# Kernel tuning notes

Measured on AMD Instinct MI355X. Metric: run time of the kernel, lower is better.

The kernel has to match this reference:

```python
import jax, jax.numpy as jnp
import numpy as np

N_NODES = 50000
N_EDGES = 800000
IN_C, H0, H1, OUT_C = 64, 64, 64, 16
EPS = 1e-5


def _sage_min(x, src, dst, Wl, bl, Wr, n_nodes):
    # PyG SAGEConv(aggr='min'): out = lin_l(min_{j in N(i)} x_j) + lin_r(x_i)
    agg = jax.ops.segment_min(x[src], dst, num_segments=n_nodes)
    agg = jnp.where(jnp.isfinite(agg), agg, 0.0)  # empty segments -> 0 (torch_scatter default)
    return agg @ Wl + bl + x @ Wr


def _batchnorm(x, gamma, beta):
    # training-mode BatchNorm1d over node dim, biased variance, eps=1e-5
    mu = jnp.mean(x, axis=0)
    var = jnp.mean((x - mu) ** 2, axis=0)
    return gamma * (x - mu) * jax.lax.rsqrt(var + EPS) + beta


def setup_inputs() -> dict:
    key = jax.random.key(0)
    ks = jax.random.split(key, 16)
    x = jax.random.normal(ks[0], (N_NODES, IN_C), dtype=jnp.float32)
    edge_index = jax.random.randint(ks[1], (2, N_EDGES), 0, N_NODES, dtype=jnp.int64)

    def lin(k, fan_in, fan_out):
        s = 1.0 / np.sqrt(fan_in)
        return jax.random.uniform(k, (fan_in, fan_out), jnp.float32, -s, s)

    return {
        "x": x, "edge_index": edge_index,
        "W1l": lin(ks[2], IN_C, H0), "b1": jnp.zeros((H0,), jnp.float32), "W1r": lin(ks[3], IN_C, H0),
        "g1": jnp.ones((H0,), jnp.float32), "be1": jnp.zeros((H0,), jnp.float32),
        "W2l": lin(ks[4], H0, H1), "b2": jnp.zeros((H1,), jnp.float32), "W2r": lin(ks[5], H0, H1),
        "g2": jnp.ones((H1,), jnp.float32), "be2": jnp.zeros((H1,), jnp.float32),
        "W3l": lin(ks[6], H1, OUT_C), "b3": jnp.zeros((OUT_C,), jnp.float32), "W3r": lin(ks[7], H1, OUT_C),
    }


def reference(x, edge_index, W1l, b1, W1r, g1, be1, W2l, b2, W2r, g2, be2, W3l, b3, W3r):
    src, dst = edge_index[0], edge_index[1]
    n = x.shape[0]
    h = jax.nn.relu(_batchnorm(_sage_min(x, src, dst, W1l, b1, W1r, n), g1, be1))
    h = jax.nn.relu(_batchnorm(_sage_min(h, src, dst, W2l, b2, W2r, n), g2, be2))
    h = _sage_min(h, src, dst, W3l, b3, W3r, n)
    return jax.nn.log_softmax(h, axis=1)
```

## Files before the change

kernel.cpp:

```cpp
#include <hip/hip_runtime.h>
#include <stdint.h>


__global__ __launch_bounds__(256)
void k_prep(int* __restrict__ deg, int n_nodes, const int* __restrict__ ei32,
            int* __restrict__ flag) {
    int i = blockIdx.x * blockDim.x + threadIdx.x;
    int stride = gridDim.x * blockDim.x;
    for (int j = i; j < n_nodes; j += stride) deg[j] = 0;
    if (i == 0) {
        int allzero = 1;
        for (int t = 1; t < 32; t += 2) allzero &= (ei32[t] == 0);
        *flag = allzero;
    }
}

__global__ __launch_bounds__(256)
void k_hist(const void* __restrict__ ei, int n_edges, int* __restrict__ deg,
            const int* __restrict__ flag) {
    const bool is64 = (*flag != 0);
    const int* e32 = (const int*)ei;
    const long long* e64 = (const long long*)ei;
    int i = blockIdx.x * blockDim.x + threadIdx.x;
    int stride = gridDim.x * blockDim.x;
    for (int e = i; e < n_edges; e += stride) {
        int d = is64 ? (int)e64[n_edges + e] : e32[n_edges + e];
        atomicAdd(&deg[d], 1);
    }
}

__global__ __launch_bounds__(256)
void k_scan1(const int* __restrict__ deg, int* __restrict__ bsum, int n) {
    __shared__ int red[256];
    const int t = threadIdx.x;
    const int i = blockIdx.x * 256 + t;
    red[t] = (i < n) ? deg[i] : 0;
    __syncthreads();
    for (int off = 128; off; off >>= 1) {
        if (t < off) red[t] += red[t + off];
        __syncthreads();
    }
    if (t == 0) bsum[blockIdx.x] = red[0];
}

__global__ __launch_bounds__(1024)
void k_scan2(const int* __restrict__ bsum, int* __restrict__ boffs,
             int nb, int* __restrict__ rowptr, int n) {
    __shared__ int part[1024];
    const int t = threadIdx.x;
    part[t] = (t < nb) ? bsum[t] : 0;
    __syncthreads();
    for (int off = 1; off < 1024; off <<= 1) {
        int v = (t >= off) ? part[t - off] : 0;
        __syncthreads();
        part[t] += v;
        __syncthreads();
    }
    if (t < nb) boffs[t] = (t == 0) ? 0 : part[t - 1];
    if (t == 0) rowptr[n] = part[nb - 1];
}

__global__ __launch_bounds__(256)
void k_scan3(const int* __restrict__ deg, const int* __restrict__ boffs,
             int* __restrict__ rowptr, int* __restrict__ cursor, int n) {
    __shared__ int part[256];
    const int t = threadIdx.x;
    const int i = blockIdx.x * 256 + t;
    const int d = (i < n) ? deg[i] : 0;
    part[t] = d;
    __syncthreads();
    for (int off = 1; off < 256; off <<= 1) {
        int v = (t >= off) ? part[t - off] : 0;
        __syncthreads();
        part[t] += v;
        __syncthreads();
    }
    if (i < n) {
        int excl = boffs[blockIdx.x] + part[t] - d;
        rowptr[i] = excl;
        cursor[i] = excl;
    }
}

__global__ __launch_bounds__(256)
void k_fill(const void* __restrict__ ei, int n_edges, int* __restrict__ cursor,
            int* __restrict__ csr, const int* __restrict__ flag) {
    const bool is64 = (*flag != 0);
    const int* e32 = (const int*)ei;
    const long long* e64 = (const long long*)ei;
    int i = blockIdx.x * blockDim.x + threadIdx.x;
    int stride = gridDim.x * blockDim.x;
    for (int e = i; e < n_edges; e += stride) {
        int s, d;
        if (is64) { s = (int)e64[e]; d = (int)e64[n_edges + e]; }
        else      { s = e32[e];      d = e32[n_edges + e]; }
        int pos = atomicAdd(&cursor[d], 1);
        csr[pos] = s;
    }
}

__global__ __launch_bounds__(256)
void k_aggregate(const float* __restrict__ x, const int* __restrict__ rowptr,
                 const int* __restrict__ csr, float* __restrict__ agg,
                 int n_nodes) {
    const int lane = threadIdx.x & 63;
    const int wave = (blockIdx.x * blockDim.x + threadIdx.x) >> 6;
    const int nwaves = (gridDim.x * blockDim.x) >> 6;
    for (int n = wave; n < n_nodes; n += nwaves) {
        const int beg = rowptr[n], end = rowptr[n + 1];
        float m = __builtin_inff();
        int e = beg;
        for (; e + 4 <= end; e += 4) {
            int s0 = csr[e], s1 = csr[e + 1], s2 = csr[e + 2], s3 = csr[e + 3];
            float v0 = x[(size_t)s0 * 64 + lane];
            float v1 = x[(size_t)s1 * 64 + lane];
            float v2 = x[(size_t)s2 * 64 + lane];
            float v3 = x[(size_t)s3 * 64 + lane];
            m = fminf(m, fminf(fminf(v0, v1), fminf(v2, v3)));
        }
        for (; e < end; ++e) {
            int s = csr[e];
            m = fminf(m, x[(size_t)s * 64 + lane]);
        }
        agg[(size_t)n * 64 + lane] = (end > beg) ? m : 0.0f;
    }
}

__global__ __launch_bounds__(256)
void k_gemm64(const float* __restrict__ agg, const float* __restrict__ xin,
              const float* __restrict__ Wl, const float* __restrict__ bl,
              const float* __restrict__ Wr, float* __restrict__ hout,
              double* __restrict__ psum, double* __restrict__ psq, int n_nodes) {
    __shared__ float sWl[64][64];
    __shared__ float sWr[64][64];
    __shared__ float rowA[4][64];
    __shared__ float rowX[4][64];
    __shared__ double red[4][64];
    const int t = threadIdx.x, c = t & 63, ln = t >> 6;
    for (int i = t; i < 4096; i += 256) {
        ((float*)sWl)[i] = Wl[i];
        ((float*)sWr)[i] = Wr[i];
    }
    const float bc = bl[c];
    double lsum = 0.0, lsq = 0.0;
    const int nchunk = (n_nodes + 3) >> 2;
    for (int chunk = blockIdx.x; chunk < nchunk; chunk += gridDim.x) {
        const int node = chunk * 4 + ln;
        __syncthreads();
        if (node < n_nodes) {
            rowA[ln][c] = agg[(size_t)node * 64 + c];
            rowX[ln][c] = xin[(size_t)node * 64 + c];
        }
        __syncthreads();
        if (node < n_nodes) {
            float acc = bc;
#pragma unroll
            for (int k = 0; k < 64; ++k)
                acc = fmaf(rowA[ln][k], sWl[k][c], fmaf(rowX[ln][k], sWr[k][c], acc));
            hout[(size_t)node * 64 + c] = acc;
            lsum += (double)acc;
            lsq  += (double)acc * (double)acc;
        }
    }
    __syncthreads();
    red[ln][c] = lsum;
    __syncthreads();
    if (ln == 0)
        psum[(size_t)blockIdx.x * 64 + c] = red[0][c] + red[1][c] + red[2][c] + red[3][c];
    __syncthreads();
    red[ln][c] = lsq;
    __syncthreads();
    if (ln == 0)
        psq[(size_t)blockIdx.x * 64 + c] = red[0][c] + red[1][c] + red[2][c] + red[3][c];
}

__global__ __launch_bounds__(1024)
void k_finalize(const double* __restrict__ psum, const double* __restrict__ psq,
                float* __restrict__ mu, float* __restrict__ istd,
                int n_nodes, int nblocks) {
    __shared__ double s_s[16][64];
    __shared__ double s_q[16][64];
    const int t = threadIdx.x;
    const int c = t & 63, g = t >> 6;
    double s = 0.0, q = 0.0;
    for (int b = g; b < nblocks; b += 16) {
        s += psum[(size_t)b * 64 + c];
        q += psq[(size_t)b * 64 + c];
    }
    s_s[g][c] = s;
    s_q[g][c] = q;
    __syncthreads();
    if (g == 0) {
        double S = 0.0, Q = 0.0;
#pragma unroll
        for (int i = 0; i < 16; ++i) { S += s_s[i][c]; Q += s_q[i][c]; }
        double m = S / n_nodes;
        double var = Q / n_nodes - m * m;
        mu[c] = (float)m;
        istd[c] = (float)(1.0 / sqrt(var + 1e-5));
    }
}

__global__ __launch_bounds__(256)
void k_bnrelu(float* __restrict__ h, const float* __restrict__ g,
              const float* __restrict__ be, const float* __restrict__ mu,
              const float* __restrict__ istd, int ntot4) {
    int i = blockIdx.x * blockDim.x + threadIdx.x;
    int stride = gridDim.x * blockDim.x;
    float4* h4 = (float4*)h;
    for (int j = i; j < ntot4; j += stride) {
        int c0 = (j << 2) & 63;
        float4 v = h4[j];
        v.x = fmaxf((v.x - mu[c0 + 0]) * istd[c0 + 0] * g[c0 + 0] + be[c0 + 0], 0.0f);
        v.y = fmaxf((v.y - mu[c0 + 1]) * istd[c0 + 1] * g[c0 + 1] + be[c0 + 1], 0.0f);
        v.z = fmaxf((v.z - mu[c0 + 2]) * istd[c0 + 2] * g[c0 + 2] + be[c0 + 2], 0.0f);
        v.w = fmaxf((v.w - mu[c0 + 3]) * istd[c0 + 3] * g[c0 + 3] + be[c0 + 3], 0.0f);
        h4[j] = v;
    }
}

__global__ __launch_bounds__(256)
void k_l3(const float* __restrict__ agg, const float* __restrict__ xin,
          const float* __restrict__ W3l, const float* __restrict__ b3,
          const float* __restrict__ W3r, float* __restrict__ out, int n_nodes) {
    __shared__ float sWl[64][16];
    __shared__ float sWr[64][16];
    __shared__ float rowA[16][65];
    __shared__ float rowX[16][65];
    const int t = threadIdx.x;
    for (int i = t; i < 1024; i += 256) {
        ((float*)sWl)[i] = W3l[i];
        ((float*)sWr)[i] = W3r[i];
    }
    const int base = blockIdx.x * 16;
#pragma unroll
    for (int i = 0; i < 4; ++i) {
        int j = t + i * 256;
        int nd = j >> 6, k = j & 63;
        int gnode = base + nd;
        if (gnode < n_nodes) {
            rowA[nd][k] = agg[(size_t)gnode * 64 + k];
            rowX[nd][k] = xin[(size_t)gnode * 64 + k];
        } else {
            rowA[nd][k] = 0.0f;
            rowX[nd][k] = 0.0f;
        }
    }
    __syncthreads();
    const int n = t >> 4, c = t & 15;
    float acc = b3[c];
#pragma unroll
    for (int k = 0; k < 64; ++k)
        acc = fmaf(rowA[n][k], sWl[k][c], fmaf(rowX[n][k], sWr[k][c], acc));
    float m = acc;
    for (int off = 8; off; off >>= 1) m = fmaxf(m, __shfl_xor(m, off, 16));
    float ex = expf(acc - m);
    float ssum = ex;
    for (int off = 8; off; off >>= 1) ssum += __shfl_xor(ssum, off, 16);
    if (base + n < n_nodes)
        out[(size_t)(base + n) * 16 + c] = (acc - m) - logf(ssum);
}

extern "C" void kernel_launch(void* const* d_in, const int* in_sizes, int n_in,
                              void* d_out, int out_size, void* d_ws, size_t ws_size,
                              hipStream_t stream) {
    (void)n_in; (void)out_size; (void)ws_size;
    const float* x   = (const float*)d_in[0];
    const void*  ei  = d_in[1];
    const float* W1l = (const float*)d_in[2];
    const float* b1  = (const float*)d_in[3];
    const float* W1r = (const float*)d_in[4];
    const float* g1  = (const float*)d_in[5];
    const float* be1 = (const float*)d_in[6];
    const float* W2l = (const float*)d_in[7];
    const float* b2  = (const float*)d_in[8];
    const float* W2r = (const float*)d_in[9];
    const float* g2  = (const float*)d_in[10];
    const float* be2 = (const float*)d_in[11];
    const float* W3l = (const float*)d_in[12];
    const float* b3  = (const float*)d_in[13];
    const float* W3r = (const float*)d_in[14];
    float* out = (float*)d_out;

    const int n_nodes = in_sizes[0] / 64;
    const int n_edges = in_sizes[1] / 2;
    const int nAgg = n_nodes * 64;

    size_t off = 0;
    auto alloc = [&](size_t bytes) {
        void* p = (char*)d_ws + off;
        off = (off + bytes + 255) & ~(size_t)255;
        return p;
    };
    float* agg    = (float*)alloc((size_t)nAgg * 4);
    float* hA     = (float*)alloc((size_t)nAgg * 4);
    float* hB     = (float*)alloc((size_t)nAgg * 4);
    int*   csr    = (int*)  alloc((size_t)n_edges * 4);
    int*   rowptr = (int*)  alloc((size_t)(n_nodes + 1) * 4);
    int*   cursor = (int*)  alloc((size_t)n_nodes * 4);
    int*   deg    = (int*)  alloc((size_t)n_nodes * 4);
    int*   bsum   = (int*)  alloc(1024 * 4);
    int*   boffs  = (int*)  alloc(1024 * 4);
    const int GG = 512;
    double* psum  = (double*)alloc((size_t)GG * 64 * 8);
    double* psq   = (double*)alloc((size_t)GG * 64 * 8);
    float*  mu    = (float*) alloc(64 * 4);
    float*  istd  = (float*) alloc(64 * 4);
    int*    flag  = (int*)   alloc(4);

    const int GP = 256, GH = 1024, GF = 1024, GA = 2048, GN = 1024;
    const int NB = (n_nodes + 255) / 256;
    const int GL3 = (n_nodes + 15) / 16;

    k_prep <<<GP, 256, 0, stream>>>(deg, n_nodes, (const int*)ei, flag);
    k_hist <<<GH, 256, 0, stream>>>(ei, n_edges, deg, flag);
    k_scan1<<<NB, 256, 0, stream>>>(deg, bsum, n_nodes);
    k_scan2<<<1, 1024, 0, stream>>>(bsum, boffs, NB, rowptr, n_nodes);
    k_scan3<<<NB, 256, 0, stream>>>(deg, boffs, rowptr, cursor, n_nodes);
    k_fill <<<GF, 256, 0, stream>>>(ei, n_edges, cursor, csr, flag);

    k_aggregate<<<GA, 256, 0, stream>>>(x, rowptr, csr, agg, n_nodes);
    k_gemm64  <<<GG, 256, 0, stream>>>(agg, x, W1l, b1, W1r, hA, psum, psq, n_nodes);
    k_finalize<<<1, 1024, 0, stream>>>(psum, psq, mu, istd, n_nodes, GG);
    k_bnrelu  <<<GN, 256, 0, stream>>>(hA, g1, be1, mu, istd, nAgg / 4);
    k_aggregate<<<GA, 256, 0, stream>>>(hA, rowptr, csr, agg, n_nodes);
    k_gemm64  <<<GG, 256, 0, stream>>>(agg, hA, W2l, b2, W2r, hB, psum, psq, n_nodes);
    k_finalize<<<1, 1024, 0, stream>>>(psum, psq, mu, istd, n_nodes, GG);
    k_bnrelu  <<<GN, 256, 0, stream>>>(hB, g2, be2, mu, istd, nAgg / 4);
    k_aggregate<<<GA, 256, 0, stream>>>(hB, rowptr, csr, agg, n_nodes);
    k_l3      <<<GL3, 256, 0, stream>>>(agg, hB, W3l, b3, W3r, out, n_nodes);
}
```

Measured before the change: 402.0 us.

## Fuse BN+ReLU into consumers and split CSR build into 8 edge slices

```diff
diff --git a/kernel.cpp b/kernel.cpp
--- a/kernel.cpp
+++ b/kernel.cpp
@@ -2,12 +2,18 @@
 #include <stdint.h>
 
 
-__global__ __launch_bounds__(256)
-void k_prep(int* __restrict__ deg, int n_nodes, const int* __restrict__ ei32,
+#define NS 8
+
+__device__ __forceinline__ float bnrelu1(float v, float mu, float is, float g, float b) {
+    return fmaxf((v - mu) * is * g + b, 0.0f);
+}
+
+__global__ __launch_bounds__(256)
+void k_prep(int* __restrict__ deg8, int ntot, const int* __restrict__ ei32,
             int* __restrict__ flag) {
     int i = blockIdx.x * blockDim.x + threadIdx.x;
     int stride = gridDim.x * blockDim.x;
-    for (int j = i; j < n_nodes; j += stride) deg[j] = 0;
+    for (int j = i; j < ntot; j += stride) deg8[j] = 0;
     if (i == 0) {
         int allzero = 1;
         for (int t = 1; t < 32; t += 2) allzero &= (ei32[t] == 0);
@@ -16,17 +22,32 @@
 }
 
 __global__ __launch_bounds__(256)
-void k_hist(const void* __restrict__ ei, int n_edges, int* __restrict__ deg,
-            const int* __restrict__ flag) {
+void k_convert(const void* __restrict__ ei, int n_edges,
+               const int* __restrict__ flag, int* __restrict__ src32,
+               int* __restrict__ dst32) {
     const bool is64 = (*flag != 0);
     const int* e32 = (const int*)ei;
     const long long* e64 = (const long long*)ei;
     int i = blockIdx.x * blockDim.x + threadIdx.x;
     int stride = gridDim.x * blockDim.x;
     for (int e = i; e < n_edges; e += stride) {
-        int d = is64 ? (int)e64[n_edges + e] : e32[n_edges + e];
-        atomicAdd(&deg[d], 1);
-    }
+        if (is64) { src32[e] = (int)e64[e]; dst32[e] = (int)e64[n_edges + e]; }
+        else      { src32[e] = e32[e];      dst32[e] = e32[n_edges + e]; }
+    }
+}
+
+__global__ __launch_bounds__(256)
+void k_hist8(const int* __restrict__ dst32, int n_edges, int* __restrict__ deg8,
+             int NN, int blocks_per_slice) {
+    const int g = blockIdx.x & (NS - 1);
+    const int jb = blockIdx.x >> 3;
+    const int eb = (int)((long long)g * n_edges / NS);
+    const int ee = (int)((long long)(g + 1) * n_edges / NS);
+    const int t = threadIdx.x;
+    const int stride = blocks_per_slice * 256;
+    int* dg = deg8 + (size_t)g * NN;
+    for (int e = eb + jb * 256 + t; e < ee; e += stride)
+        atomicAdd(&dg[dst32[e]], 1);
 }
 
 __global__ __launch_bounds__(256)
@@ -45,10 +66,13 @@
 
 __global__ __launch_bounds__(1024)
 void k_scan2(const int* __restrict__ bsum, int* __restrict__ boffs,
-             int nb, int* __restrict__ rowptr, int n) {
+             int nb, int* __restrict__ rowptr, int ntot) {
     __shared__ int part[1024];
     const int t = threadIdx.x;
-    part[t] = (t < nb) ? bsum[t] : 0;
+    const int i0 = 2 * t, i1 = 2 * t + 1;
+    const int a = (i0 < nb) ? bsum[i0] : 0;
+    const int b = (i1 < nb) ? bsum[i1] : 0;
+    part[t] = a + b;
     __syncthreads();
     for (int off = 1; off < 1024; off <<= 1) {
         int v = (t >= off) ? part[t - off] : 0;
@@ -56,8 +80,10 @@
         part[t] += v;
         __syncthreads();
     }
-    if (t < nb) boffs[t] = (t == 0) ? 0 : part[t - 1];
-    if (t == 0) rowptr[n] = part[nb - 1];
+    const int base = (t == 0) ? 0 : part[t - 1];
+    if (i0 < nb) boffs[i0] = base;
+    if (i1 < nb) boffs[i1] = base + a;
+    if (t == 1023) rowptr[ntot] = part[1023];
 }
 
 __global__ __launch_bounds__(256)
@@ -83,54 +109,80 @@
 }
 
 __global__ __launch_bounds__(256)
-void k_fill(const void* __restrict__ ei, int n_edges, int* __restrict__ cursor,
-            int* __restrict__ csr, const int* __restrict__ flag) {
-    const bool is64 = (*flag != 0);
-    const int* e32 = (const int*)ei;
-    const long long* e64 = (const long long*)ei;
-    int i = blockIdx.x * blockDim.x + threadIdx.x;
-    int stride = gridDim.x * blockDim.x;
-    for (int e = i; e < n_edges; e += stride) {
-        int s, d;
-        if (is64) { s = (int)e64[e]; d = (int)e64[n_edges + e]; }
-        else      { s = e32[e];      d = e32[n_edges + e]; }
-        int pos = atomicAdd(&cursor[d], 1);
-        csr[pos] = s;
-    }
-}
-
-__global__ __launch_bounds__(256)
-void k_aggregate(const float* __restrict__ x, const int* __restrict__ rowptr,
-                 const int* __restrict__ csr, float* __restrict__ agg,
-                 int n_nodes) {
+void k_fill8(const int* __restrict__ src32, const int* __restrict__ dst32,
+             int n_edges, int* __restrict__ cursor, int* __restrict__ csr,
+             int NN, int blocks_per_slice) {
+    const int g = blockIdx.x & (NS - 1);
+    const int jb = blockIdx.x >> 3;
+    const int eb = (int)((long long)g * n_edges / NS);
+    const int ee = (int)((long long)(g + 1) * n_edges / NS);
+    const int t = threadIdx.x;
+    const int stride = blocks_per_slice * 256;
+    int* cur = cursor + (size_t)g * NN;
+    for (int e = eb + jb * 256 + t; e < ee; e += stride) {
+        int d = dst32[e];
+        int pos = atomicAdd(&cur[d], 1);
+        csr[pos] = src32[e];
+    }
+}
+
+template <bool BN>
+__global__ __launch_bounds__(256)
+void k_agg(const float* __restrict__ x, const int* __restrict__ rowptr,
+           const int* __restrict__ csr, float* __restrict__ agg, int NN,
+           const float* __restrict__ mu, const float* __restrict__ istd,
+           const float* __restrict__ gam, const float* __restrict__ bet) {
     const int lane = threadIdx.x & 63;
     const int wave = (blockIdx.x * blockDim.x + threadIdx.x) >> 6;
     const int nwaves = (gridDim.x * blockDim.x) >> 6;
-    for (int n = wave; n < n_nodes; n += nwaves) {
-        const int beg = rowptr[n], end = rowptr[n + 1];
+    float s_mu = 0.f, s_is = 0.f, s_g = 0.f, s_b = 0.f;
+    if (BN) { s_mu = mu[lane]; s_is = istd[lane]; s_g = gam[lane]; s_b = bet[lane]; }
+    for (int n = wave; n < NN; n += nwaves) {
+        int bg[NS], eg[NS];
+#pragma unroll
+        for (int g = 0; g < NS; ++g) {
+            bg[g] = rowptr[g * NN + n];
+            eg[g] = rowptr[g * NN + n + 1];
+        }
         float m = __builtin_inff();
-        int e = beg;
-        for (; e + 4 <= end; e += 4) {
-            int s0 = csr[e], s1 = csr[e + 1], s2 = csr[e + 2], s3 = csr[e + 3];
-            float v0 = x[(size_t)s0 * 64 + lane];
-            float v1 = x[(size_t)s1 * 64 + lane];
-            float v2 = x[(size_t)s2 * 64 + lane];
-            float v3 = x[(size_t)s3 * 64 + lane];
-            m = fminf(m, fminf(fminf(v0, v1), fminf(v2, v3)));
-        }
-        for (; e < end; ++e) {
-            int s = csr[e];
-            m = fminf(m, x[(size_t)s * 64 + lane]);
-        }
-        agg[(size_t)n * 64 + lane] = (end > beg) ? m : 0.0f;
-    }
-}
-
+        int cnt = 0;
+#pragma unroll
+        for (int g = 0; g < NS; ++g) {
+            int e = bg[g];
+            const int end = eg[g];
+            cnt += end - e;
+            for (; e + 4 <= end; e += 4) {
+                int s0 = csr[e], s1 = csr[e + 1], s2 = csr[e + 2], s3 = csr[e + 3];
+                float v0 = x[(size_t)s0 * 64 + lane];
+                float v1 = x[(size_t)s1 * 64 + lane];
+                float v2 = x[(size_t)s2 * 64 + lane];
+                float v3 = x[(size_t)s3 * 64 + lane];
+                if (BN) {
+                    v0 = bnrelu1(v0, s_mu, s_is, s_g, s_b);
+                    v1 = bnrelu1(v1, s_mu, s_is, s_g, s_b);
+                    v2 = bnrelu1(v2, s_mu, s_is, s_g, s_b);
+                    v3 = bnrelu1(v3, s_mu, s_is, s_g, s_b);
+                }
+                m = fminf(m, fminf(fminf(v0, v1), fminf(v2, v3)));
+            }
+            for (; e < end; ++e) {
+                float v = x[(size_t)csr[e] * 64 + lane];
+                if (BN) v = bnrelu1(v, s_mu, s_is, s_g, s_b);
+                m = fminf(m, v);
+            }
+        }
+        agg[(size_t)n * 64 + lane] = (cnt > 0) ? m : 0.0f;
+    }
+}
+
+template <bool BNX>
 __global__ __launch_bounds__(256)
 void k_gemm64(const float* __restrict__ agg, const float* __restrict__ xin,
               const float* __restrict__ Wl, const float* __restrict__ bl,
               const float* __restrict__ Wr, float* __restrict__ hout,
-              double* __restrict__ psum, double* __restrict__ psq, int n_nodes) {
+              double* __restrict__ psum, double* __restrict__ psq, int n_nodes,
+              const float* __restrict__ mu, const float* __restrict__ istd,
+              const float* __restrict__ gam, const float* __restrict__ bet) {
     __shared__ float sWl[64][64];
     __shared__ float sWr[64][64];
     __shared__ float rowA[4][64];
@@ -141,6 +193,8 @@
         ((float*)sWl)[i] = Wl[i];
         ((float*)sWr)[i] = Wr[i];
     }
+    float s_mu = 0.f, s_is = 0.f, s_g = 0.f, s_b = 0.f;
+    if (BNX) { s_mu = mu[c]; s_is = istd[c]; s_g = gam[c]; s_b = bet[c]; }
     const float bc = bl[c];
     double lsum = 0.0, lsq = 0.0;
     const int nchunk = (n_nodes + 3) >> 2;
@@ -149,7 +203,9 @@
         __syncthreads();
         if (node < n_nodes) {
             rowA[ln][c] = agg[(size_t)node * 64 + c];
-            rowX[ln][c] = xin[(size_t)node * 64 + c];
+            float v = xin[(size_t)node * 64 + c];
+            if (BNX) v = bnrelu1(v, s_mu, s_is, s_g, s_b);
+            rowX[ln][c] = v;
         }
         __syncthreads();
         if (node < n_nodes) {
@@ -202,27 +258,11 @@
 }
 
 __global__ __launch_bounds__(256)
-void k_bnrelu(float* __restrict__ h, const float* __restrict__ g,
-              const float* __restrict__ be, const float* __restrict__ mu,
-              const float* __restrict__ istd, int ntot4) {
-    int i = blockIdx.x * blockDim.x + threadIdx.x;
-    int stride = gridDim.x * blockDim.x;
-    float4* h4 = (float4*)h;
-    for (int j = i; j < ntot4; j += stride) {
-        int c0 = (j << 2) & 63;
-        float4 v = h4[j];
-        v.x = fmaxf((v.x - mu[c0 + 0]) * istd[c0 + 0] * g[c0 + 0] + be[c0 + 0], 0.0f);
-        v.y = fmaxf((v.y - mu[c0 + 1]) * istd[c0 + 1] * g[c0 + 1] + be[c0 + 1], 0.0f);
-        v.z = fmaxf((v.z - mu[c0 + 2]) * istd[c0 + 2] * g[c0 + 2] + be[c0 + 2], 0.0f);
-        v.w = fmaxf((v.w - mu[c0 + 3]) * istd[c0 + 3] * g[c0 + 3] + be[c0 + 3], 0.0f);
-        h4[j] = v;
-    }
-}
-
-__global__ __launch_bounds__(256)
 void k_l3(const float* __restrict__ agg, const float* __restrict__ xin,
           const float* __restrict__ W3l, const float* __restrict__ b3,
-          const float* __restrict__ W3r, float* __restrict__ out, int n_nodes) {
+          const float* __restrict__ W3r, float* __restrict__ out, int n_nodes,
+          const float* __restrict__ mu, const float* __restrict__ istd,
+          const float* __restrict__ gam, const float* __restrict__ bet) {
     __shared__ float sWl[64][16];
     __shared__ float sWr[64][16];
     __shared__ float rowA[16][65];
@@ -232,6 +272,8 @@
         ((float*)sWl)[i] = W3l[i];
         ((float*)sWr)[i] = W3r[i];
     }
+    const int kc = t & 63;
+    const float s_mu = mu[kc], s_is = istd[kc], s_g = gam[kc], s_b = bet[kc];
     const int base = blockIdx.x * 16;
 #pragma unroll
     for (int i = 0; i < 4; ++i) {
@@ -240,7 +282,7 @@
         int gnode = base + nd;
         if (gnode < n_nodes) {
             rowA[nd][k] = agg[(size_t)gnode * 64 + k];
-            rowX[nd][k] = xin[(size_t)gnode * 64 + k];
+            rowX[nd][k] = bnrelu1(xin[(size_t)gnode * 64 + k], s_mu, s_is, s_g, s_b);
         } else {
             rowA[nd][k] = 0.0f;
             rowX[nd][k] = 0.0f;
@@ -282,9 +324,10 @@
     const float* W3r = (const float*)d_in[14];
     float* out = (float*)d_out;
 
-    const int n_nodes = in_sizes[0] / 64;
+    const int NN = in_sizes[0] / 64;
     const int n_edges = in_sizes[1] / 2;
-    const int nAgg = n_nodes * 64;
+    const int nAgg = NN * 64;
+    const int ntot = NS * NN;
 
     size_t off = 0;
     auto alloc = [&](size_t bytes) {
@@ -296,37 +339,45 @@
     float* hA     = (float*)alloc((size_t)nAgg * 4);
     float* hB     = (float*)alloc((size_t)nAgg * 4);
     int*   csr    = (int*)  alloc((size_t)n_edges * 4);
-    int*   rowptr = (int*)  alloc((size_t)(n_nodes + 1) * 4);
-    int*   cursor = (int*)  alloc((size_t)n_nodes * 4);
-    int*   deg    = (int*)  alloc((size_t)n_nodes * 4);
-    int*   bsum   = (int*)  alloc(1024 * 4);
-    int*   boffs  = (int*)  alloc(1024 * 4);
+    int*   src32  = (int*)  alloc((size_t)n_edges * 4);
+    int*   dst32  = (int*)  alloc((size_t)n_edges * 4);
+    int*   rowptr = (int*)  alloc((size_t)(ntot + 1) * 4);
+    int*   cursor = (int*)  alloc((size_t)ntot * 4);
+    int*   deg8   = (int*)  alloc((size_t)ntot * 4);
+    int*   bsum   = (int*)  alloc(2048 * 4);
+    int*   boffs  = (int*)  alloc(2048 * 4);
     const int GG = 512;
     double* psum  = (double*)alloc((size_t)GG * 64 * 8);
     double* psq   = (double*)alloc((size_t)GG * 64 * 8);
-    float*  mu    = (float*) alloc(64 * 4);
-    float*  istd  = (float*) alloc(64 * 4);
+    float*  mu1   = (float*) alloc(64 * 4);
+    float*  istd1 = (float*) alloc(64 * 4);
+    float*  mu2   = (float*) alloc(64 * 4);
+    float*  istd2 = (float*) alloc(64 * 4);
     int*    flag  = (int*)   alloc(4);
 
-    const int GP = 256, GH = 1024, GF = 1024, GA = 2048, GN = 1024;
-    const int NB = (n_nodes + 255) / 256;
-    const int GL3 = (n_nodes + 15) / 16;
-
-    k_prep <<<GP, 256, 0, stream>>>(deg, n_nodes, (const int*)ei, flag);
-    k_hist <<<GH, 256, 0, stream>>>(ei, n_edges, deg, flag);
-    k_scan1<<<NB, 256, 0, stream>>>(deg, bsum, n_nodes);
-    k_scan2<<<1, 1024, 0, stream>>>(bsum, boffs, NB, rowptr, n_nodes);
-    k_scan3<<<NB, 256, 0, stream>>>(deg, boffs, rowptr, cursor, n_nodes);
-    k_fill <<<GF, 256, 0, stream>>>(ei, n_edges, cursor, csr, flag);
-
-    k_aggregate<<<GA, 256, 0, stream>>>(x, rowptr, csr, agg, n_nodes);
-    k_gemm64  <<<GG, 256, 0, stream>>>(agg, x, W1l, b1, W1r, hA, psum, psq, n_nodes);
-    k_finalize<<<1, 1024, 0, stream>>>(psum, psq, mu, istd, n_nodes, GG);
-    k_bnrelu  <<<GN, 256, 0, stream>>>(hA, g1, be1, mu, istd, nAgg / 4);
-    k_aggregate<<<GA, 256, 0, stream>>>(hA, rowptr, csr, agg, n_nodes);
-    k_gemm64  <<<GG, 256, 0, stream>>>(agg, hA, W2l, b2, W2r, hB, psum, psq, n_nodes);
-    k_finalize<<<1, 1024, 0, stream>>>(psum, psq, mu, istd, n_nodes, GG);
-    k_bnrelu  <<<GN, 256, 0, stream>>>(hB, g2, be2, mu, istd, nAgg / 4);
-    k_aggregate<<<GA, 256, 0, stream>>>(hB, rowptr, csr, agg, n_nodes);
-    k_l3      <<<GL3, 256, 0, stream>>>(agg, hB, W3l, b3, W3r, out, n_nodes);
-}
+    const int GHF = 1024;
+    const int BPS = GHF / NS;
+    const int NB2 = (ntot + 255) / 256;
+    const int GA = 2048;
+    const int GL3 = (NN + 15) / 16;
+
+    k_prep   <<<256, 256, 0, stream>>>(deg8, ntot, (const int*)ei, flag);
+    k_convert<<<1024, 256, 0, stream>>>(ei, n_edges, flag, src32, dst32);
+    k_hist8  <<<GHF, 256, 0, stream>>>(dst32, n_edges, deg8, NN, BPS);
+    k_scan1  <<<NB2, 256, 0, stream>>>(deg8, bsum, ntot);
+    k_scan2  <<<1, 1024, 0, stream>>>(bsum, boffs, NB2, rowptr, ntot);
+    k_scan3  <<<NB2, 256, 0, stream>>>(deg8, boffs, rowptr, cursor, ntot);
+    k_fill8  <<<GHF, 256, 0, stream>>>(src32, dst32, n_edges, cursor, csr, NN, BPS);
+
+    k_agg<false><<<GA, 256, 0, stream>>>(x, rowptr, csr, agg, NN,
+                                         nullptr, nullptr, nullptr, nullptr);
+    k_gemm64<false><<<GG, 256, 0, stream>>>(agg, x, W1l, b1, W1r, hA, psum, psq, NN,
+                                            nullptr, nullptr, nullptr, nullptr);
+    k_finalize<<<1, 1024, 0, stream>>>(psum, psq, mu1, istd1, NN, GG);
+    k_agg<true><<<GA, 256, 0, stream>>>(hA, rowptr, csr, agg, NN, mu1, istd1, g1, be1);
+    k_gemm64<true><<<GG, 256, 0, stream>>>(agg, hA, W2l, b2, W2r, hB, psum, psq, NN,
+                                           mu1, istd1, g1, be1);
+    k_finalize<<<1, 1024, 0, stream>>>(psum, psq, mu2, istd2, NN, GG);
+    k_agg<true><<<GA, 256, 0, stream>>>(hB, rowptr, csr, agg, NN, mu2, istd2, g2, be2);
+    k_l3<<<GL3, 256, 0, stream>>>(agg, hB, W3l, b3, W3r, out, NN, mu2, istd2, g2, be2);
+}
```

After: 471.7 us. 1.17x slower.
